# Optimization experiments

Hardware: AMD Instinct MI355X
Metric: run time of the kernel (lower is better)

## Reference

```python
import jax, jax.numpy as jnp
import numpy as np

PHI = 1.618033988749895  # golden ratio
LUT_SIZE = 4096
TWO_PI = 2.0 * float(np.pi)
_grid = np.arange(LUT_SIZE, dtype=np.float32) * (TWO_PI / LUT_SIZE)
SIN_TABLE = jnp.asarray(np.sin(_grid).astype(np.float32))
COS_TABLE = jnp.asarray(np.cos(_grid).astype(np.float32))


def lut_sin_cos(theta):
    """4096-entry sin/cos lookup table over [0, 2pi) with linear interpolation."""
    pos = theta * (LUT_SIZE / TWO_PI)
    i0 = jnp.floor(pos)
    frac = (pos - i0).astype(theta.dtype)
    idx0 = jnp.mod(i0.astype(jnp.int32), LUT_SIZE)
    idx1 = jnp.mod(idx0 + 1, LUT_SIZE)
    sin_v = SIN_TABLE[idx0] * (1.0 - frac) + SIN_TABLE[idx1] * frac
    cos_v = COS_TABLE[idx0] * (1.0 - frac) + COS_TABLE[idx1] * frac
    return sin_v, cos_v


def _forward(input_ids, emb, w_query, b_query, w_key, b_key, w_ctx, W_res, B_res, w_pr, w_pi, w_out):
    B, S = input_ids.shape
    D = emb.shape[1] // 2
    H, dh = w_query.shape
    e = emb[input_ids]                               # [B,S,2D]
    w_emb, b_emb = e[..., :D], e[..., D:]
    t_arr = jnp.arange(S, dtype=jnp.float32)

    # --- sequential euler-transform recurrence (the only truly serial part) ---
    def step(carry, xs):
        h_r, h_i = carry
        w_t, b_t, t = xs                             # [B,D],[B,D],scalar
        wl = 1.0 + jnp.abs(w_t)
        tp = t * PHI
        th_r = h_r / wl + b_t + tp
        th_i = h_i / wl + b_t + tp
        sr, cr = lut_sin_cos(th_r)
        si, ci = lut_sin_cos(th_i)
        nr = cr * ci - sr * si
        ni = cr * si + sr * ci
        return (nr, ni), nr + ni

    init = (jnp.zeros((B, D), dtype=emb.dtype), jnp.zeros((B, D), dtype=emb.dtype))
    xs = (jnp.swapaxes(w_emb, 0, 1), jnp.swapaxes(b_emb, 0, 1), t_arr)
    _, states = jax.lax.scan(step, init, xs)         # [S,B,D]
    states = jnp.swapaxes(states, 0, 1)              # [B,S,D] == cached_states

    # --- multi-head LUT sin/cos attention over strictly-previous cached states ---
    xp = states.reshape(B, S, H, dh)                 # per-head patches
    t_phi = t_arr * PHI                              # [S]
    th_q = xp / (1.0 + jnp.abs(w_query)) + b_query + t_phi[None, :, None, None]
    sq, cq = lut_sin_cos(th_q)
    q = jnp.concatenate([cq, sq], axis=-1)           # [B,S,H,2dh]
    th_k = xp / (1.0 + jnp.abs(w_key)) + b_key
    sk, ck = lut_sin_cos(th_k)
    k = jnp.concatenate([ck, sk], axis=-1)           # [B,S,H,2dh]
    scale = float(np.sqrt(2.0 * dh))
    scores = jnp.einsum('bthd,bshd->bhts', q, k) / scale
    mask = jnp.tril(jnp.ones((S, S), dtype=bool), k=-1)   # keys strictly before query
    scores = jnp.where(mask[None, None], scores, -1e30)
    weights = jax.nn.softmax(scores, axis=-1)
    context = jnp.einsum('bhts,bsd->btd', weights, states)   # heads summed
    has_ctx = (t_arr > 0).astype(states.dtype)[None, :, None]  # t=0 has no cache
    x = states + has_ctx * (context @ w_ctx.T)

    # --- resonant layer over num_neurons ---
    wl_res = 1.0 + jnp.abs(W_res)                    # [N,D]
    theta = x[:, :, None, :] / wl_res + B_res + t_phi[None, :, None, None]  # [B,S,N,D]
    s_t, c_t = lut_sin_cos(theta)
    cos_sum = c_t.sum(-1)                            # [B,S,N]
    sin_sum = s_t.sum(-1)
    x = x + jax.nn.silu(cos_sum @ w_pr.T + sin_sum @ w_pi.T)

    return x @ w_out.T                               # [B,S,V]


def setup_inputs() -> dict:
    key = jax.random.key(0)
    ks = jax.random.split(key, 12)
    B, S, V, D, H, N = 8, 512, 32000, 64, 4, 128
    dh = D // H
    return {
        'input_ids': jax.random.randint(ks[0], (B, S), 0, V),
        'emb': jax.random.normal(ks[1], (V, 2 * D), dtype=jnp.float32) * 0.02,
        'w_query': jax.random.normal(ks[2], (H, dh), dtype=jnp.float32) * 0.02,
        'b_query': jnp.zeros((H, dh), dtype=jnp.float32),
        'w_key': jax.random.normal(ks[3], (H, dh), dtype=jnp.float32) * 0.02,
        'b_key': jnp.zeros((H, dh), dtype=jnp.float32),
        'w_ctx': jax.random.normal(ks[4], (D, D), dtype=jnp.float32) * 0.02,
        'W_res': jax.random.normal(ks[5], (N, D), dtype=jnp.float32) * 0.02,
        'B_res': jnp.zeros((N, D), dtype=jnp.float32),
        'w_pr': jax.random.normal(ks[6], (D, N), dtype=jnp.float32) * 0.02,
        'w_pi': jax.random.normal(ks[7], (D, N), dtype=jnp.float32) * 0.02,
        'w_out': jax.random.normal(ks[8], (V, D), dtype=jnp.float32) * 0.02,
    }


def reference(input_ids, emb, w_query, b_query, w_key, b_key, w_ctx, W_res, B_res, w_pr, w_pi, w_out):
    return _forward(input_ids, emb, w_query, b_query, w_key, b_key, w_ctx, W_res, B_res, w_pr, w_pi, w_out)
```

## Files before the change

kernel.cpp:

```cpp
#include <hip/hip_runtime.h>
#include <hip/hip_bf16.h>
#include <math.h>

#define PHI_F     1.618033988749895f
#define LUT_N     4096
#define LUT_INV   651.8986469044033f
#define LUT_STEP  0.0015339807878856412f

#define B_  8
#define S_  512
#define D_  64
#define H_  4
#define DH_ 16
#define N_  128
#define V_  32000
#define R_  (B_ * S_)

typedef __attribute__((ext_vector_type(8))) short short8_t;
typedef __attribute__((ext_vector_type(4))) float f32x4;

__device__ __forceinline__ void lut2(const float2* __restrict__ sc,
                                     float th, float& s, float& c) {
    float pos = th * LUT_INV;
    float f0  = floorf(pos);
    float fr  = pos - f0;
    int   i0  = ((int)f0) & (LUT_N - 1);
    int   i1  = (i0 + 1) & (LUT_N - 1);
    float2 p0 = sc[i0];
    float2 p1 = sc[i1];
    float om  = 1.0f - fr;
    s = p0.x * om + p1.x * fr;
    c = p0.y * om + p1.y * fr;
}

__global__ void k_tables(float2* __restrict__ scT) {
    int i = blockIdx.x * blockDim.x + threadIdx.x;
    if (i < LUT_N) {
        float g = (float)i * LUT_STEP;
        scT[i] = make_float2((float)sin((double)g), (float)cos((double)g));
    }
}

__global__ __launch_bounds__(256) void k_cvt(const float* __restrict__ w,
                                             __hip_bfloat16* __restrict__ wb,
                                             int n4) {
    int i = blockIdx.x * 256 + threadIdx.x;
    if (i < n4) {
        float4 v = ((const float4*)w)[i];
        union { __hip_bfloat16 h[4]; short4 s4; } u;
        u.h[0] = __float2bfloat16(v.x);
        u.h[1] = __float2bfloat16(v.y);
        u.h[2] = __float2bfloat16(v.z);
        u.h[3] = __float2bfloat16(v.w);
        *(short4*)(&wb[4 * i]) = u.s4;
    }
}

__global__ __launch_bounds__(256) void k_wpre(const float* __restrict__ Wres,
                                              const float* __restrict__ Bres,
                                              const float* __restrict__ wpr,
                                              const float* __restrict__ wpi,
                                              float2* __restrict__ ibres,
                                              float2* __restrict__ wpT) {
    int idx = blockIdx.x * 256 + threadIdx.x;
    if (idx < N_ * D_) {
        ibres[idx] = make_float2(1.0f / (1.0f + fabsf(Wres[idx])), Bres[idx]);
        int nn = idx >> 6, d = idx & 63;
        wpT[idx] = make_float2(wpr[d * N_ + nn], wpi[d * N_ + nn]);
    }
}

__global__ __launch_bounds__(256) void k_pre(const int* __restrict__ ids,
                                             const float* __restrict__ emb,
                                             float2* __restrict__ wlbt) {
    int idx = blockIdx.x * 256 + threadIdx.x;
    int d  = idx & (D_ - 1);
    int bt = idx >> 6;
    int id = ids[bt];
    float w = emb[(size_t)id * (2 * D_) + d];
    float b = emb[(size_t)id * (2 * D_) + D_ + d];
    wlbt[idx] = make_float2(1.0f + fabsf(w), b);
}

__global__ __launch_bounds__(64) void k_scan(const float2* __restrict__ wlbt,
                                             const float2* __restrict__ scT,
                                             float* __restrict__ states) {
    __shared__ float2 sc[LUT_N];
    int d = threadIdx.x;
    int b = blockIdx.x;
    for (int i = d; i < LUT_N; i += 64) sc[i] = scT[i];
    __syncthreads();

    const float2* src  = wlbt + (size_t)b * S_ * D_ + d;
    float*        outp = states + (size_t)b * S_ * D_ + d;

    float2 cur[8], nxt[8];
#pragma unroll
    for (int j = 0; j < 8; ++j) cur[j] = src[j * D_];

    float hr = 0.0f, hi = 0.0f;
    for (int tc = 0; tc < S_; tc += 8) {
        int tn = (tc + 8) & (S_ - 1);
#pragma unroll
        for (int j = 0; j < 8; ++j) nxt[j] = src[(tn + j) * D_];
#pragma unroll
        for (int j = 0; j < 8; ++j) {
            int   t   = tc + j;
            float wl  = cur[j].x;
            float btv = cur[j].y;
            float tp  = (float)t * PHI_F;
            float thr = hr / wl + btv + tp;
            float thi = hi / wl + btv + tp;
            float sr, cr, si, ci;
            lut2(sc, thr, sr, cr);
            lut2(sc, thi, si, ci);
            float nr = cr * ci - sr * si;
            float ni = cr * si + sr * ci;
            hr = nr; hi = ni;
            outp[t * D_] = nr + ni;
        }
#pragma unroll
        for (int j = 0; j < 8; ++j) cur[j] = nxt[j];
    }
}

__global__ __launch_bounds__(256) void k_qk(const float* __restrict__ states,
                                            const float* __restrict__ wq,
                                            const float* __restrict__ bq,
                                            const float* __restrict__ wk,
                                            const float* __restrict__ bk,
                                            const float2* __restrict__ scT,
                                            float* __restrict__ q,
                                            float* __restrict__ kT) {
    __shared__ float2 sc[LUT_N];
    for (int i = threadIdx.x; i < LUT_N; i += 256) sc[i] = scT[i];
    __syncthreads();
    const int total = R_ * H_ * DH_;
    for (int idx = blockIdx.x * 256 + threadIdx.x; idx < total; idx += gridDim.x * 256) {
        int j  = idx & (DH_ - 1);
        int h  = (idx >> 4) & (H_ - 1);
        int bt = idx >> 6;
        int t  = bt & (S_ - 1);
        int b  = bt >> 9;
        float xp = states[idx];
        float tp = (float)t * PHI_F;
        int   hj = h * DH_ + j;
        float thq = xp / (1.0f + fabsf(wq[hj])) + bq[hj] + tp;
        float thk = xp / (1.0f + fabsf(wk[hj])) + bk[hj];
        float sq, cq, sk, ck;
        lut2(sc, thq, sq, cq);
        lut2(sc, thk, sk, ck);
        int base = bt * (H_ * 2 * DH_) + h * (2 * DH_) + j;
        q[base] = cq; q[base + DH_] = sq;
        size_t kb = ((size_t)(b * H_ + h) * 32 + j) * S_ + t;
        kT[kb] = ck; kT[kb + 16 * S_] = sk;
    }
}

__global__ __launch_bounds__(256) void k_attn(const float* __restrict__ states,
                                              const float* __restrict__ q,
                                              const float* __restrict__ kT,
                                              const float* __restrict__ wctx,
                                              float* __restrict__ x) {
    int bt = blockIdx.x;
    int b  = bt >> 9, t = bt & (S_ - 1);
    int tid = threadIdx.x;
    if (t == 0) {
        if (tid < D_) x[bt * D_ + tid] = states[bt * D_ + tid];
        return;
    }
    __shared__ float wlds[H_][S_];
    __shared__ float ql[H_][2 * DH_];
    __shared__ float cpart[4][D_];
    int h = tid >> 6, l = tid & 63;
    if (l < 2 * DH_) ql[h][l] = q[bt * 128 + h * 32 + l];
    __syncthreads();

    const float* kTb = kT + (size_t)(b * H_ + h) * 32 * S_;
    float sc[8];
    float m = -INFINITY;
#pragma unroll
    for (int jj = 0; jj < 8; ++jj) {
        int s = l + jj * 64;
        float v = -INFINITY;
        if (s < t) {
            float acc = 0.0f;
#pragma unroll
            for (int c = 0; c < 32; ++c)
                acc = fmaf(kTb[c * S_ + s], ql[h][c], acc);
            v = acc * 0.1767766952966369f;
            m = fmaxf(m, v);
        }
        sc[jj] = v;
    }
    for (int o = 32; o; o >>= 1) m = fmaxf(m, __shfl_xor(m, o));
    float sum = 0.0f;
#pragma unroll
    for (int jj = 0; jj < 8; ++jj) {
        float e = __expf(sc[jj] - m);
        sc[jj] = e; sum += e;
    }
    for (int o = 32; o; o >>= 1) sum += __shfl_xor(sum, o);
    float inv = 1.0f / sum;
#pragma unroll
    for (int jj = 0; jj < 8; ++jj) {
        int s = l + jj * 64;
        if (s < S_) wlds[h][s] = sc[jj] * inv;
    }
    __syncthreads();
    {
        int d = tid & 63, p = tid >> 6;
        float acc = 0.0f;
        for (int s = p; s < t; s += 4) {
            float w4 = wlds[0][s] + wlds[1][s] + wlds[2][s] + wlds[3][s];
            acc += w4 * states[((size_t)b * S_ + s) * D_ + d];
        }
        cpart[p][d] = acc;
    }
    __syncthreads();
    if (tid < D_) {
        float c = cpart[0][tid] + cpart[1][tid] + cpart[2][tid] + cpart[3][tid];
        cpart[0][tid] = c;
    }
    __syncthreads();
    if (tid < D_) {
        float y = 0.0f;
        const float* wr = wctx + tid * D_;
        for (int d = 0; d < D_; ++d) y += cpart[0][d] * wr[d];
        x[bt * D_ + tid] = states[bt * D_ + tid] + y;
    }
}

__global__ __launch_bounds__(256) void k_resid(const float* __restrict__ x,
                                               const float2* __restrict__ ibres,
                                               const float2* __restrict__ wpT,
                                               const float2* __restrict__ scT,
                                               __hip_bfloat16* __restrict__ xb) {
    __shared__ float2 sc[LUT_N];
    __shared__ float xv[D_];
    __shared__ float csum[N_], ssum[N_];
    __shared__ float part[4][D_];
    int tid = threadIdx.x;
    for (int i = tid; i < LUT_N; i += 256) sc[i] = scT[i];
    int n  = tid >> 1;
    int d0 = (tid & 1) * 32;
    float2 ib[32];
#pragma unroll
    for (int dd = 0; dd < 32; ++dd) ib[dd] = ibres[n * D_ + d0 + dd];
    int g = tid >> 6, dl = tid & 63;
    for (int r = 0; r < 8; ++r) {
        int bt = blockIdx.x * 8 + r;
        int t  = bt & (S_ - 1);
        float tp = (float)t * PHI_F;
        __syncthreads();
        if (tid < D_) xv[tid] = x[bt * D_ + tid];
        __syncthreads();
        float cs = 0.0f, ss = 0.0f;
#pragma unroll
        for (int dd = 0; dd < 32; ++dd) {
            float th = fmaf(xv[d0 + dd], ib[dd].x, ib[dd].y) + tp;
            float s, c;
            lut2(sc, th, s, c);
            cs += c; ss += s;
        }
        cs += __shfl_xor(cs, 1);
        ss += __shfl_xor(ss, 1);
        if ((tid & 1) == 0) { csum[n] = cs; ssum[n] = ss; }
        __syncthreads();
        float acc = 0.0f;
#pragma unroll
        for (int nn = 0; nn < 32; ++nn) {
            float2 w = wpT[(g * 32 + nn) * D_ + dl];
            acc = fmaf(csum[g * 32 + nn], w.x, fmaf(ssum[g * 32 + nn], w.y, acc));
        }
        part[g][dl] = acc;
        __syncthreads();
        if (tid < D_) {
            float pre = part[0][tid] + part[1][tid] + part[2][tid] + part[3][tid];
            float sig = 1.0f / (1.0f + __expf(-pre));
            xb[bt * D_ + tid] = __float2bfloat16(xv[tid] + pre * sig);
        }
    }
}

__global__ __launch_bounds__(256) void k_out(const __hip_bfloat16* __restrict__ xb,
                                             const __hip_bfloat16* __restrict__ wb,
                                             float* __restrict__ out) {
    __shared__ float ot[64][132];
    int tid  = threadIdx.x;
    int wave = tid >> 6, l = tid & 63;
    int wr = wave >> 1, wc = wave & 1;
    int m0 = blockIdx.y * 64 + wr * 32;
    int r  = l & 15;
    int ks = (l >> 4) * 8;
    int kh = l >> 4;

    short8_t a[2][2];
#pragma unroll
    for (int mi = 0; mi < 2; ++mi)
#pragma unroll
        for (int kk = 0; kk < 2; ++kk)
            a[mi][kk] = *reinterpret_cast<const short8_t*>(
                xb + (size_t)(m0 + mi * 16 + r) * 64 + kk * 32 + ks);

    for (int ch = 0; ch < 2; ++ch) {
        int c0 = blockIdx.x * 256 + ch * 128 + wc * 64;
        short8_t b[4][2];
#pragma unroll
        for (int ni = 0; ni < 4; ++ni)
#pragma unroll
            for (int kk = 0; kk < 2; ++kk)
                b[ni][kk] = *reinterpret_cast<const short8_t*>(
                    wb + (size_t)(c0 + ni * 16 + r) * 64 + kk * 32 + ks);

        f32x4 acc[2][4];
#pragma unroll
        for (int mi = 0; mi < 2; ++mi)
#pragma unroll
            for (int ni = 0; ni < 4; ++ni) {
                acc[mi][ni] = (f32x4){0.f, 0.f, 0.f, 0.f};
                acc[mi][ni] = __builtin_amdgcn_mfma_f32_16x16x32_bf16(
                    a[mi][0], b[ni][0], acc[mi][ni], 0, 0, 0);
                acc[mi][ni] = __builtin_amdgcn_mfma_f32_16x16x32_bf16(
                    a[mi][1], b[ni][1], acc[mi][ni], 0, 0, 0);
            }

        if (ch) __syncthreads();
#pragma unroll
        for (int mi = 0; mi < 2; ++mi)
#pragma unroll
            for (int ni = 0; ni < 4; ++ni)
#pragma unroll
                for (int i = 0; i < 4; ++i)
                    ot[wr * 32 + mi * 16 + kh * 4 + i][wc * 64 + ni * 16 + r] = acc[mi][ni][i];
        __syncthreads();

        size_t rbase = blockIdx.y * 64;
        size_t cb    = (size_t)blockIdx.x * 256 + ch * 128;
#pragma unroll
        for (int j = 0; j < 8; ++j) {
            int idx = j * 256 + tid;
            int row = idx >> 5, c4 = idx & 31;
            float4 v = *(const float4*)&ot[row][c4 * 4];
            *(float4*)&out[(rbase + row) * V_ + cb + c4 * 4] = v;
        }
    }
}

extern "C" void kernel_launch(void* const* d_in, const int* in_sizes, int n_in,
                              void* d_out, int out_size, void* d_ws, size_t ws_size,
                              hipStream_t stream) {
    const int*   ids  = (const int*)  d_in[0];
    const float* emb  = (const float*)d_in[1];
    const float* wq   = (const float*)d_in[2];
    const float* bq   = (const float*)d_in[3];
    const float* wk   = (const float*)d_in[4];
    const float* bk   = (const float*)d_in[5];
    const float* wctx = (const float*)d_in[6];
    const float* Wres = (const float*)d_in[7];
    const float* Bres = (const float*)d_in[8];
    const float* wpr  = (const float*)d_in[9];
    const float* wpi  = (const float*)d_in[10];
    const float* wout = (const float*)d_in[11];
    float* out = (float*)d_out;

    float* states = (float*)d_ws;
    float* qbuf   = states + R_ * D_;
    float* kTbuf  = qbuf + R_ * 128;
    float* xbuf   = kTbuf + B_ * H_ * 32 * S_;
    __hip_bfloat16* wb = (__hip_bfloat16*)(xbuf + R_ * D_);
    __hip_bfloat16* xb = wb + (size_t)V_ * D_;
    float2* scT   = (float2*)(xb + R_ * D_);
    float2* wlbt  = scT + LUT_N;
    float2* ibres = wlbt + R_ * D_;
    float2* wpT   = ibres + N_ * D_;

    k_tables<<<16, 256, 0, stream>>>(scT);
    k_cvt   <<<(V_ * D_ / 4 + 255) / 256, 256, 0, stream>>>(wout, wb, V_ * D_ / 4);
    k_wpre  <<<(N_ * D_ + 255) / 256, 256, 0, stream>>>(Wres, Bres, wpr, wpi, ibres, wpT);
    k_pre   <<<R_ * D_ / 256, 256, 0, stream>>>(ids, emb, wlbt);
    k_scan  <<<B_, 64, 0, stream>>>(wlbt, scT, states);
    k_qk    <<<64, 256, 0, stream>>>(states, wq, bq, wk, bk, scT, qbuf, kTbuf);
    k_attn  <<<R_, 256, 0, stream>>>(states, qbuf, kTbuf, wctx, xbuf);
    k_resid <<<R_ / 8, 256, 0, stream>>>(xbuf, ibres, wpT, scT, xb);
    k_out   <<<dim3(V_ / 256, R_ / 64), 256, 0, stream>>>(xb, wb, out);
}
```

Baseline: 359.9 us.

## Fuse preprocessing, scan, and QK into one kernel; merge attention with residual

```diff
diff --git a/kernel.cpp b/kernel.cpp
--- a/kernel.cpp
+++ b/kernel.cpp
@@ -41,73 +41,69 @@
     }
 }
 
-__global__ __launch_bounds__(256) void k_cvt(const float* __restrict__ w,
-                                             __hip_bfloat16* __restrict__ wb,
-                                             int n4) {
-    int i = blockIdx.x * 256 + threadIdx.x;
-    if (i < n4) {
-        float4 v = ((const float4*)w)[i];
-        union { __hip_bfloat16 h[4]; short4 s4; } u;
-        u.h[0] = __float2bfloat16(v.x);
-        u.h[1] = __float2bfloat16(v.y);
-        u.h[2] = __float2bfloat16(v.z);
-        u.h[3] = __float2bfloat16(v.w);
-        *(short4*)(&wb[4 * i]) = u.s4;
-    }
-}
-
-__global__ __launch_bounds__(256) void k_wpre(const float* __restrict__ Wres,
-                                              const float* __restrict__ Bres,
-                                              const float* __restrict__ wpr,
-                                              const float* __restrict__ wpi,
-                                              float2* __restrict__ ibres,
-                                              float2* __restrict__ wpT) {
-    int idx = blockIdx.x * 256 + threadIdx.x;
-    if (idx < N_ * D_) {
-        ibres[idx] = make_float2(1.0f / (1.0f + fabsf(Wres[idx])), Bres[idx]);
-        int nn = idx >> 6, d = idx & 63;
-        wpT[idx] = make_float2(wpr[d * N_ + nn], wpi[d * N_ + nn]);
-    }
-}
-
-__global__ __launch_bounds__(256) void k_pre(const int* __restrict__ ids,
-                                             const float* __restrict__ emb,
-                                             float2* __restrict__ wlbt) {
-    int idx = blockIdx.x * 256 + threadIdx.x;
-    int d  = idx & (D_ - 1);
-    int bt = idx >> 6;
-    int id = ids[bt];
-    float w = emb[(size_t)id * (2 * D_) + d];
-    float b = emb[(size_t)id * (2 * D_) + D_ + d];
-    wlbt[idx] = make_float2(1.0f + fabsf(w), b);
-}
-
-__global__ __launch_bounds__(64) void k_scan(const float2* __restrict__ wlbt,
-                                             const float2* __restrict__ scT,
-                                             float* __restrict__ states) {
+__global__ __launch_bounds__(256) void k_fused0(
+        const int* __restrict__ ids, const float* __restrict__ emb,
+        const float* __restrict__ wq, const float* __restrict__ bq,
+        const float* __restrict__ wk, const float* __restrict__ bk,
+        const float* __restrict__ Wres, const float* __restrict__ Bres,
+        const float* __restrict__ wpr, const float* __restrict__ wpi,
+        const float* __restrict__ wout, const float2* __restrict__ scT,
+        float* __restrict__ states, float* __restrict__ q, float* __restrict__ kT,
+        __hip_bfloat16* __restrict__ wb, float2* __restrict__ ibres,
+        float2* __restrict__ wpT) {
+    int blk = blockIdx.x;
+    int tid = threadIdx.x;
+    if (blk >= 8) {
+        if (blk < 2008) {
+            int i = (blk - 8) * 256 + tid;
+            float4 v = ((const float4*)wout)[i];
+            union { __hip_bfloat16 h[4]; short4 s4; } u;
+            u.h[0] = __float2bfloat16(v.x);
+            u.h[1] = __float2bfloat16(v.y);
+            u.h[2] = __float2bfloat16(v.z);
+            u.h[3] = __float2bfloat16(v.w);
+            *(short4*)(&wb[4 * (size_t)i]) = u.s4;
+        } else {
+            int idx = (blk - 2008) * 256 + tid;
+            ibres[idx] = make_float2(1.0f / (1.0f + fabsf(Wres[idx])), Bres[idx]);
+            int nn = idx >> 6, d = idx & 63;
+            wpT[idx] = make_float2(wpr[d * N_ + nn], wpi[d * N_ + nn]);
+        }
+        return;
+    }
     __shared__ float2 sc[LUT_N];
-    int d = threadIdx.x;
-    int b = blockIdx.x;
-    for (int i = d; i < LUT_N; i += 64) sc[i] = scT[i];
-    __syncthreads();
-
-    const float2* src  = wlbt + (size_t)b * S_ * D_ + d;
-    float*        outp = states + (size_t)b * S_ * D_ + d;
-
-    float2 cur[8], nxt[8];
-#pragma unroll
-    for (int j = 0; j < 8; ++j) cur[j] = src[j * D_];
-
+    __shared__ int idsh[S_];
+    for (int i = tid; i < LUT_N; i += 256) sc[i] = scT[i];
+    for (int i = tid; i < S_; i += 256) idsh[i] = ids[blk * S_ + i];
+    __syncthreads();
+    if (tid >= 64) return;
+    int d = tid, b = blk;
+    float cw[8], cb[8], nw[8], nb[8];
+#pragma unroll
+    for (int j = 0; j < 8; ++j) {
+        int id = idsh[j];
+        cw[j] = emb[(size_t)id * 128 + d];
+        cb[j] = emb[(size_t)id * 128 + 64 + d];
+    }
+    float* outp = states + (size_t)b * S_ * D_ + d;
+    float* qp   = q + (size_t)b * S_ * 128;
+    int h = d >> 4, j4 = d & 15, hj = h * DH_ + j4;
+    float wlq = 1.0f + fabsf(wq[hj]); float bqv = bq[hj];
+    float wlk = 1.0f + fabsf(wk[hj]); float bkv = bk[hj];
+    float* kTp = kT + ((size_t)(b * H_ + h) * 32 + j4) * S_;
     float hr = 0.0f, hi = 0.0f;
     for (int tc = 0; tc < S_; tc += 8) {
-        int tn = (tc + 8) & (S_ - 1);
-#pragma unroll
-        for (int j = 0; j < 8; ++j) nxt[j] = src[(tn + j) * D_];
-#pragma unroll
-        for (int j = 0; j < 8; ++j) {
-            int   t   = tc + j;
-            float wl  = cur[j].x;
-            float btv = cur[j].y;
+#pragma unroll
+        for (int jj = 0; jj < 8; ++jj) {
+            int id = idsh[(tc + 8 + jj) & (S_ - 1)];
+            nw[jj] = emb[(size_t)id * 128 + d];
+            nb[jj] = emb[(size_t)id * 128 + 64 + d];
+        }
+#pragma unroll
+        for (int jj = 0; jj < 8; ++jj) {
+            int   t   = tc + jj;
+            float wl  = 1.0f + fabsf(cw[jj]);
+            float btv = cb[jj];
             float tp  = (float)t * PHI_F;
             float thr = hr / wl + btv + tp;
             float thi = hi / wl + btv + tp;
@@ -117,176 +113,139 @@
             float nr = cr * ci - sr * si;
             float ni = cr * si + sr * ci;
             hr = nr; hi = ni;
-            outp[t * D_] = nr + ni;
-        }
-#pragma unroll
-        for (int j = 0; j < 8; ++j) cur[j] = nxt[j];
-    }
-}
-
-__global__ __launch_bounds__(256) void k_qk(const float* __restrict__ states,
-                                            const float* __restrict__ wq,
-                                            const float* __restrict__ bq,
-                                            const float* __restrict__ wk,
-                                            const float* __restrict__ bk,
+            float xp = nr + ni;
+            outp[t * D_] = xp;
+            float thq = xp / wlq + bqv + tp;
+            float thk = xp / wlk + bkv;
+            float sq, cq, sk, ck;
+            lut2(sc, thq, sq, cq);
+            lut2(sc, thk, sk, ck);
+            float* qrow = qp + t * 128 + h * 32 + j4;
+            qrow[0]  = cq; qrow[16] = sq;
+            kTp[t] = ck; kTp[16 * S_ + t] = sk;
+        }
+#pragma unroll
+        for (int jj = 0; jj < 8; ++jj) { cw[jj] = nw[jj]; cb[jj] = nb[jj]; }
+    }
+}
+
+__global__ __launch_bounds__(256) void k_ar(const float* __restrict__ states,
+                                            const float* __restrict__ q,
+                                            const float* __restrict__ kT,
+                                            const float* __restrict__ wctx,
+                                            const float2* __restrict__ ibres,
+                                            const float2* __restrict__ wpT,
                                             const float2* __restrict__ scT,
-                                            float* __restrict__ q,
-                                            float* __restrict__ kT) {
+                                            __hip_bfloat16* __restrict__ xb) {
     __shared__ float2 sc[LUT_N];
-    for (int i = threadIdx.x; i < LUT_N; i += 256) sc[i] = scT[i];
-    __syncthreads();
-    const int total = R_ * H_ * DH_;
-    for (int idx = blockIdx.x * 256 + threadIdx.x; idx < total; idx += gridDim.x * 256) {
-        int j  = idx & (DH_ - 1);
-        int h  = (idx >> 4) & (H_ - 1);
-        int bt = idx >> 6;
-        int t  = bt & (S_ - 1);
-        int b  = bt >> 9;
-        float xp = states[idx];
-        float tp = (float)t * PHI_F;
-        int   hj = h * DH_ + j;
-        float thq = xp / (1.0f + fabsf(wq[hj])) + bq[hj] + tp;
-        float thk = xp / (1.0f + fabsf(wk[hj])) + bk[hj];
-        float sq, cq, sk, ck;
-        lut2(sc, thq, sq, cq);
-        lut2(sc, thk, sk, ck);
-        int base = bt * (H_ * 2 * DH_) + h * (2 * DH_) + j;
-        q[base] = cq; q[base + DH_] = sq;
-        size_t kb = ((size_t)(b * H_ + h) * 32 + j) * S_ + t;
-        kT[kb] = ck; kT[kb + 16 * S_] = sk;
-    }
-}
-
-__global__ __launch_bounds__(256) void k_attn(const float* __restrict__ states,
-                                              const float* __restrict__ q,
-                                              const float* __restrict__ kT,
-                                              const float* __restrict__ wctx,
-                                              float* __restrict__ x) {
+    __shared__ float wlds[H_][S_];
+    __shared__ float ql[H_][2 * DH_];
+    __shared__ float cpart[4][D_];
+    __shared__ float xv[D_];
+    __shared__ float csum[N_], ssum[N_];
+    __shared__ float part[4][D_];
     int bt = blockIdx.x;
     int b  = bt >> 9, t = bt & (S_ - 1);
     int tid = threadIdx.x;
-    if (t == 0) {
-        if (tid < D_) x[bt * D_ + tid] = states[bt * D_ + tid];
-        return;
-    }
-    __shared__ float wlds[H_][S_];
-    __shared__ float ql[H_][2 * DH_];
-    __shared__ float cpart[4][D_];
     int h = tid >> 6, l = tid & 63;
-    if (l < 2 * DH_) ql[h][l] = q[bt * 128 + h * 32 + l];
-    __syncthreads();
-
-    const float* kTb = kT + (size_t)(b * H_ + h) * 32 * S_;
-    float sc[8];
-    float m = -INFINITY;
-#pragma unroll
-    for (int jj = 0; jj < 8; ++jj) {
-        int s = l + jj * 64;
-        float v = -INFINITY;
-        if (s < t) {
-            float acc = 0.0f;
-#pragma unroll
-            for (int c = 0; c < 32; ++c)
-                acc = fmaf(kTb[c * S_ + s], ql[h][c], acc);
-            v = acc * 0.1767766952966369f;
-            m = fmaxf(m, v);
-        }
-        sc[jj] = v;
-    }
-    for (int o = 32; o; o >>= 1) m = fmaxf(m, __shfl_xor(m, o));
-    float sum = 0.0f;
-#pragma unroll
-    for (int jj = 0; jj < 8; ++jj) {
-        float e = __expf(sc[jj] - m);
-        sc[jj] = e; sum += e;
-    }
-    for (int o = 32; o; o >>= 1) sum += __shfl_xor(sum, o);
-    float inv = 1.0f / sum;
-#pragma unroll
-    for (int jj = 0; jj < 8; ++jj) {
-        int s = l + jj * 64;
-        if (s < S_) wlds[h][s] = sc[jj] * inv;
-    }
-    __syncthreads();
-    {
-        int d = tid & 63, p = tid >> 6;
+    for (int i = tid; i < LUT_N; i += 256) sc[i] = scT[i];
+    if (t > 0 && l < 2 * DH_) ql[h][l] = q[bt * 128 + h * 32 + l];
+    __syncthreads();
+
+    if (t > 0) {
+        const float* kTb = kT + (size_t)(b * H_ + h) * 32 * S_;
+        float scv[8];
+        float m = -INFINITY;
+#pragma unroll
+        for (int jj = 0; jj < 8; ++jj) {
+            int s = l + jj * 64;
+            float v = -INFINITY;
+            if (s < t) {
+                float acc = 0.0f;
+#pragma unroll
+                for (int c = 0; c < 32; ++c)
+                    acc = fmaf(kTb[c * S_ + s], ql[h][c], acc);
+                v = acc * 0.1767766952966369f;
+                m = fmaxf(m, v);
+            }
+            scv[jj] = v;
+        }
+        for (int o = 32; o; o >>= 1) m = fmaxf(m, __shfl_xor(m, o));
+        float sum = 0.0f;
+#pragma unroll
+        for (int jj = 0; jj < 8; ++jj) {
+            float e = __expf(scv[jj] - m);
+            scv[jj] = e; sum += e;
+        }
+        for (int o = 32; o; o >>= 1) sum += __shfl_xor(sum, o);
+        float inv = 1.0f / sum;
+#pragma unroll
+        for (int jj = 0; jj < 8; ++jj) {
+            int s = l + jj * 64;
+            if (s < S_) wlds[h][s] = scv[jj] * inv;
+        }
+    }
+    __syncthreads();
+    if (t > 0) {
+        int dd = tid & 63, p = tid >> 6;
         float acc = 0.0f;
         for (int s = p; s < t; s += 4) {
             float w4 = wlds[0][s] + wlds[1][s] + wlds[2][s] + wlds[3][s];
-            acc += w4 * states[((size_t)b * S_ + s) * D_ + d];
-        }
-        cpart[p][d] = acc;
-    }
+            acc += w4 * states[((size_t)b * S_ + s) * D_ + dd];
+        }
+        cpart[p][dd] = acc;
+    }
+    __syncthreads();
+    if (tid < D_ && t > 0)
+        cpart[0][tid] = cpart[0][tid] + cpart[1][tid] + cpart[2][tid] + cpart[3][tid];
     __syncthreads();
     if (tid < D_) {
-        float c = cpart[0][tid] + cpart[1][tid] + cpart[2][tid] + cpart[3][tid];
-        cpart[0][tid] = c;
-    }
-    __syncthreads();
-    if (tid < D_) {
-        float y = 0.0f;
-        const float* wr = wctx + tid * D_;
-        for (int d = 0; d < D_; ++d) y += cpart[0][d] * wr[d];
-        x[bt * D_ + tid] = states[bt * D_ + tid] + y;
-    }
-}
-
-__global__ __launch_bounds__(256) void k_resid(const float* __restrict__ x,
-                                               const float2* __restrict__ ibres,
-                                               const float2* __restrict__ wpT,
-                                               const float2* __restrict__ scT,
-                                               __hip_bfloat16* __restrict__ xb) {
-    __shared__ float2 sc[LUT_N];
-    __shared__ float xv[D_];
-    __shared__ float csum[N_], ssum[N_];
-    __shared__ float part[4][D_];
-    int tid = threadIdx.x;
-    for (int i = tid; i < LUT_N; i += 256) sc[i] = scT[i];
+        float base = states[bt * D_ + tid];
+        float val  = base;
+        if (t > 0) {
+            float y = 0.0f;
+            const float* wr = wctx + tid * D_;
+            for (int dd = 0; dd < D_; ++dd) y += cpart[0][dd] * wr[dd];
+            val = base + y;
+        }
+        xv[tid] = val;
+    }
+    __syncthreads();
     int n  = tid >> 1;
     int d0 = (tid & 1) * 32;
-    float2 ib[32];
-#pragma unroll
-    for (int dd = 0; dd < 32; ++dd) ib[dd] = ibres[n * D_ + d0 + dd];
+    float tp = (float)t * PHI_F;
+    float cs = 0.0f, ss = 0.0f;
+#pragma unroll
+    for (int dd = 0; dd < 32; ++dd) {
+        float2 ib = ibres[n * D_ + d0 + dd];
+        float th = fmaf(xv[d0 + dd], ib.x, ib.y) + tp;
+        float s, c;
+        lut2(sc, th, s, c);
+        cs += c; ss += s;
+    }
+    cs += __shfl_xor(cs, 1);
+    ss += __shfl_xor(ss, 1);
+    if ((tid & 1) == 0) { csum[n] = cs; ssum[n] = ss; }
+    __syncthreads();
     int g = tid >> 6, dl = tid & 63;
-    for (int r = 0; r < 8; ++r) {
-        int bt = blockIdx.x * 8 + r;
-        int t  = bt & (S_ - 1);
-        float tp = (float)t * PHI_F;
-        __syncthreads();
-        if (tid < D_) xv[tid] = x[bt * D_ + tid];
-        __syncthreads();
-        float cs = 0.0f, ss = 0.0f;
-#pragma unroll
-        for (int dd = 0; dd < 32; ++dd) {
-            float th = fmaf(xv[d0 + dd], ib[dd].x, ib[dd].y) + tp;
-            float s, c;
-            lut2(sc, th, s, c);
-            cs += c; ss += s;
-        }
-        cs += __shfl_xor(cs, 1);
-        ss += __shfl_xor(ss, 1);
-        if ((tid & 1) == 0) { csum[n] = cs; ssum[n] = ss; }
-        __syncthreads();
-        float acc = 0.0f;
-#pragma unroll
-        for (int nn = 0; nn < 32; ++nn) {
-            float2 w = wpT[(g * 32 + nn) * D_ + dl];
-            acc = fmaf(csum[g * 32 + nn], w.x, fmaf(ssum[g * 32 + nn], w.y, acc));
-        }
-        part[g][dl] = acc;
-        __syncthreads();
-        if (tid < D_) {
-            float pre = part[0][tid] + part[1][tid] + part[2][tid] + part[3][tid];
-            float sig = 1.0f / (1.0f + __expf(-pre));
-            xb[bt * D_ + tid] = __float2bfloat16(xv[tid] + pre * sig);
-        }
+    float acc = 0.0f;
+#pragma unroll
+    for (int nn = 0; nn < 32; ++nn) {
+        float2 w = wpT[(g * 32 + nn) * D_ + dl];
+        acc = fmaf(csum[g * 32 + nn], w.x, fmaf(ssum[g * 32 + nn], w.y, acc));
+    }
+    part[g][dl] = acc;
+    __syncthreads();
+    if (tid < D_) {
+        float pre = part[0][tid] + part[1][tid] + part[2][tid] + part[3][tid];
+        float sig = 1.0f / (1.0f + __expf(-pre));
+        xb[bt * D_ + tid] = __float2bfloat16(xv[tid] + pre * sig);
     }
 }
 
 __global__ __launch_bounds__(256) void k_out(const __hip_bfloat16* __restrict__ xb,
                                              const __hip_bfloat16* __restrict__ wb,
                                              float* __restrict__ out) {
-    __shared__ float ot[64][132];
     int tid  = threadIdx.x;
     int wave = tid >> 6, l = tid & 63;
     int wr = wave >> 1, wc = wave & 1;
@@ -303,14 +262,15 @@
             a[mi][kk] = *reinterpret_cast<const short8_t*>(
                 xb + (size_t)(m0 + mi * 16 + r) * 64 + kk * 32 + ks);
 
+#pragma unroll
     for (int ch = 0; ch < 2; ++ch) {
         int c0 = blockIdx.x * 256 + ch * 128 + wc * 64;
-        short8_t b[4][2];
+        short8_t bfr[4][2];
 #pragma unroll
         for (int ni = 0; ni < 4; ++ni)
 #pragma unroll
             for (int kk = 0; kk < 2; ++kk)
-                b[ni][kk] = *reinterpret_cast<const short8_t*>(
+                bfr[ni][kk] = *reinterpret_cast<const short8_t*>(
                     wb + (size_t)(c0 + ni * 16 + r) * 64 + kk * 32 + ks);
 
         f32x4 acc[2][4];
@@ -320,30 +280,20 @@
             for (int ni = 0; ni < 4; ++ni) {
                 acc[mi][ni] = (f32x4){0.f, 0.f, 0.f, 0.f};
                 acc[mi][ni] = __builtin_amdgcn_mfma_f32_16x16x32_bf16(
-                    a[mi][0], b[ni][0], acc[mi][ni], 0, 0, 0);
+                    a[mi][0], bfr[ni][0], acc[mi][ni], 0, 0, 0);
                 acc[mi][ni] = __builtin_amdgcn_mfma_f32_16x16x32_bf16(
-                    a[mi][1], b[ni][1], acc[mi][ni], 0, 0, 0);
+                    a[mi][1], bfr[ni][1], acc[mi][ni], 0, 0, 0);
             }
-
-        if (ch) __syncthreads();
 #pragma unroll
         for (int mi = 0; mi < 2; ++mi)
 #pragma unroll
-            for (int ni = 0; ni < 4; ++ni)
-#pragma unroll
-                for (int i = 0; i < 4; ++i)
-                    ot[wr * 32 + mi * 16 + kh * 4 + i][wc * 64 + ni * 16 + r] = acc[mi][ni][i];
-        __syncthreads();
-
-        size_t rbase = blockIdx.y * 64;
-        size_t cb    = (size_t)blockIdx.x * 256 + ch * 128;
-#pragma unroll
-        for (int j = 0; j < 8; ++j) {
-            int idx = j * 256 + tid;
-            int row = idx >> 5, c4 = idx & 31;
-            float4 v = *(const float4*)&ot[row][c4 * 4];
-            *(float4*)&out[(rbase + row) * V_ + cb + c4 * 4] = v;
-        }
+            for (int i = 0; i < 4; ++i) {
+                size_t rowoff = (size_t)(m0 + mi * 16 + kh * 4 + i) * V_;
+#pragma unroll
+                for (int ni = 0; ni < 4; ++ni)
+                    __builtin_nontemporal_store(acc[mi][ni][i],
+                        &out[rowoff + c0 + ni * 16 + r]);
+            }
     }
 }
 
@@ -367,21 +317,16 @@
     float* states = (float*)d_ws;
     float* qbuf   = states + R_ * D_;
     float* kTbuf  = qbuf + R_ * 128;
-    float* xbuf   = kTbuf + B_ * H_ * 32 * S_;
-    __hip_bfloat16* wb = (__hip_bfloat16*)(xbuf + R_ * D_);
+    __hip_bfloat16* wb = (__hip_bfloat16*)(kTbuf + B_ * H_ * 32 * S_);
     __hip_bfloat16* xb = wb + (size_t)V_ * D_;
     float2* scT   = (float2*)(xb + R_ * D_);
-    float2* wlbt  = scT + LUT_N;
-    float2* ibres = wlbt + R_ * D_;
+    float2* ibres = scT + LUT_N;
     float2* wpT   = ibres + N_ * D_;
 
     k_tables<<<16, 256, 0, stream>>>(scT);
-    k_cvt   <<<(V_ * D_ / 4 + 255) / 256, 256, 0, stream>>>(wout, wb, V_ * D_ / 4);
-    k_wpre  <<<(N_ * D_ + 255) / 256, 256, 0, stream>>>(Wres, Bres, wpr, wpi, ibres, wpT);
-    k_pre   <<<R_ * D_ / 256, 256, 0, stream>>>(ids, emb, wlbt);
-    k_scan  <<<B_, 64, 0, stream>>>(wlbt, scT, states);
-    k_qk    <<<64, 256, 0, stream>>>(states, wq, bq, wk, bk, scT, qbuf, kTbuf);
-    k_attn  <<<R_, 256, 0, stream>>>(states, qbuf, kTbuf, wctx, xbuf);
-    k_resid <<<R_ / 8, 256, 0, stream>>>(xbuf, ibres, wpT, scT, xb);
+    k_fused0<<<2040, 256, 0, stream>>>(ids, emb, wq, bq, wk, bk, Wres, Bres,
+                                       wpr, wpi, wout, scT,
+                                       states, qbuf, kTbuf, wb, ibres, wpT);
+    k_ar    <<<R_, 256, 0, stream>>>(states, qbuf, kTbuf, wctx, ibres, wpT, scT, xb);
     k_out   <<<dim3(V_ / 256, R_ / 64), 256, 0, stream>>>(xb, wb, out);
 }
```

New measurement: 481.3 us. 33.7% more time.

## Fuse weight conversion, residual prep and embedding gather into the scan kernel

Applied to the files above, without the earlier changes.

```diff
diff --git a/kernel.cpp b/kernel.cpp
--- a/kernel.cpp
+++ b/kernel.cpp
@@ -41,73 +41,61 @@
     }
 }
 
-__global__ __launch_bounds__(256) void k_cvt(const float* __restrict__ w,
-                                             __hip_bfloat16* __restrict__ wb,
-                                             int n4) {
-    int i = blockIdx.x * 256 + threadIdx.x;
-    if (i < n4) {
-        float4 v = ((const float4*)w)[i];
-        union { __hip_bfloat16 h[4]; short4 s4; } u;
-        u.h[0] = __float2bfloat16(v.x);
-        u.h[1] = __float2bfloat16(v.y);
-        u.h[2] = __float2bfloat16(v.z);
-        u.h[3] = __float2bfloat16(v.w);
-        *(short4*)(&wb[4 * i]) = u.s4;
-    }
-}
-
-__global__ __launch_bounds__(256) void k_wpre(const float* __restrict__ Wres,
-                                              const float* __restrict__ Bres,
-                                              const float* __restrict__ wpr,
-                                              const float* __restrict__ wpi,
-                                              float2* __restrict__ ibres,
-                                              float2* __restrict__ wpT) {
-    int idx = blockIdx.x * 256 + threadIdx.x;
-    if (idx < N_ * D_) {
-        ibres[idx] = make_float2(1.0f / (1.0f + fabsf(Wres[idx])), Bres[idx]);
-        int nn = idx >> 6, d = idx & 63;
-        wpT[idx] = make_float2(wpr[d * N_ + nn], wpi[d * N_ + nn]);
-    }
-}
-
-__global__ __launch_bounds__(256) void k_pre(const int* __restrict__ ids,
-                                             const float* __restrict__ emb,
-                                             float2* __restrict__ wlbt) {
-    int idx = blockIdx.x * 256 + threadIdx.x;
-    int d  = idx & (D_ - 1);
-    int bt = idx >> 6;
-    int id = ids[bt];
-    float w = emb[(size_t)id * (2 * D_) + d];
-    float b = emb[(size_t)id * (2 * D_) + D_ + d];
-    wlbt[idx] = make_float2(1.0f + fabsf(w), b);
-}
-
-__global__ __launch_bounds__(64) void k_scan(const float2* __restrict__ wlbt,
-                                             const float2* __restrict__ scT,
-                                             float* __restrict__ states) {
+__global__ __launch_bounds__(256) void k_fused0(
+        const int* __restrict__ ids, const float* __restrict__ emb,
+        const float* __restrict__ Wres, const float* __restrict__ Bres,
+        const float* __restrict__ wpr, const float* __restrict__ wpi,
+        const float* __restrict__ wout, const float2* __restrict__ scT,
+        float* __restrict__ states, __hip_bfloat16* __restrict__ wb,
+        float2* __restrict__ ibres, float2* __restrict__ wpT) {
+    int blk = blockIdx.x;
+    int tid = threadIdx.x;
+    if (blk >= 8) {
+        if (blk < 2008) {
+            int i = (blk - 8) * 256 + tid;
+            float4 v = ((const float4*)wout)[i];
+            union { __hip_bfloat16 h[4]; short4 s4; } u;
+            u.h[0] = __float2bfloat16(v.x);
+            u.h[1] = __float2bfloat16(v.y);
+            u.h[2] = __float2bfloat16(v.z);
+            u.h[3] = __float2bfloat16(v.w);
+            *(short4*)(&wb[4 * (size_t)i]) = u.s4;
+        } else {
+            int idx = (blk - 2008) * 256 + tid;
+            ibres[idx] = make_float2(1.0f / (1.0f + fabsf(Wres[idx])), Bres[idx]);
+            int nn = idx >> 6, d = idx & 63;
+            wpT[idx] = make_float2(wpr[d * N_ + nn], wpi[d * N_ + nn]);
+        }
+        return;
+    }
     __shared__ float2 sc[LUT_N];
-    int d = threadIdx.x;
-    int b = blockIdx.x;
-    for (int i = d; i < LUT_N; i += 64) sc[i] = scT[i];
-    __syncthreads();
-
-    const float2* src  = wlbt + (size_t)b * S_ * D_ + d;
-    float*        outp = states + (size_t)b * S_ * D_ + d;
-
-    float2 cur[8], nxt[8];
-#pragma unroll
-    for (int j = 0; j < 8; ++j) cur[j] = src[j * D_];
-
+    __shared__ int idsh[S_];
+    for (int i = tid; i < LUT_N; i += 256) sc[i] = scT[i];
+    for (int i = tid; i < S_; i += 256) idsh[i] = ids[blk * S_ + i];
+    __syncthreads();
+    if (tid >= 64) return;
+    int d = tid, b = blk;
+    float cw[8], cb[8], nw[8], nb[8];
+#pragma unroll
+    for (int j = 0; j < 8; ++j) {
+        int id = idsh[j];
+        cw[j] = emb[(size_t)id * 128 + d];
+        cb[j] = emb[(size_t)id * 128 + 64 + d];
+    }
+    float* outp = states + (size_t)b * S_ * D_ + d;
     float hr = 0.0f, hi = 0.0f;
     for (int tc = 0; tc < S_; tc += 8) {
-        int tn = (tc + 8) & (S_ - 1);
-#pragma unroll
-        for (int j = 0; j < 8; ++j) nxt[j] = src[(tn + j) * D_];
-#pragma unroll
-        for (int j = 0; j < 8; ++j) {
-            int   t   = tc + j;
-            float wl  = cur[j].x;
-            float btv = cur[j].y;
+#pragma unroll
+        for (int jj = 0; jj < 8; ++jj) {
+            int id = idsh[(tc + 8 + jj) & (S_ - 1)];
+            nw[jj] = emb[(size_t)id * 128 + d];
+            nb[jj] = emb[(size_t)id * 128 + 64 + d];
+        }
+#pragma unroll
+        for (int jj = 0; jj < 8; ++jj) {
+            int   t   = tc + jj;
+            float wl  = 1.0f + fabsf(cw[jj]);
+            float btv = cb[jj];
             float tp  = (float)t * PHI_F;
             float thr = hr / wl + btv + tp;
             float thi = hi / wl + btv + tp;
@@ -120,7 +108,7 @@
             outp[t * D_] = nr + ni;
         }
 #pragma unroll
-        for (int j = 0; j < 8; ++j) cur[j] = nxt[j];
+        for (int jj = 0; jj < 8; ++jj) { cw[jj] = nw[jj]; cb[jj] = nb[jj]; }
     }
 }
 
@@ -209,13 +197,13 @@
     }
     __syncthreads();
     {
-        int d = tid & 63, p = tid >> 6;
+        int dd = tid & 63, p = tid >> 6;
         float acc = 0.0f;
         for (int s = p; s < t; s += 4) {
             float w4 = wlds[0][s] + wlds[1][s] + wlds[2][s] + wlds[3][s];
-            acc += w4 * states[((size_t)b * S_ + s) * D_ + d];
-        }
-        cpart[p][d] = acc;
+            acc += w4 * states[((size_t)b * S_ + s) * D_ + dd];
+        }
+        cpart[p][dd] = acc;
     }
     __syncthreads();
     if (tid < D_) {
@@ -226,7 +214,7 @@
     if (tid < D_) {
         float y = 0.0f;
         const float* wr = wctx + tid * D_;
-        for (int d = 0; d < D_; ++d) y += cpart[0][d] * wr[d];
+        for (int dd = 0; dd < D_; ++dd) y += cpart[0][dd] * wr[dd];
         x[bt * D_ + tid] = states[bt * D_ + tid] + y;
     }
 }
@@ -371,15 +359,12 @@
     __hip_bfloat16* wb = (__hip_bfloat16*)(xbuf + R_ * D_);
     __hip_bfloat16* xb = wb + (size_t)V_ * D_;
     float2* scT   = (float2*)(xb + R_ * D_);
-    float2* wlbt  = scT + LUT_N;
-    float2* ibres = wlbt + R_ * D_;
+    float2* ibres = scT + LUT_N;
     float2* wpT   = ibres + N_ * D_;
 
     k_tables<<<16, 256, 0, stream>>>(scT);
-    k_cvt   <<<(V_ * D_ / 4 + 255) / 256, 256, 0, stream>>>(wout, wb, V_ * D_ / 4);
-    k_wpre  <<<(N_ * D_ + 255) / 256, 256, 0, stream>>>(Wres, Bres, wpr, wpi, ibres, wpT);
-    k_pre   <<<R_ * D_ / 256, 256, 0, stream>>>(ids, emb, wlbt);
-    k_scan  <<<B_, 64, 0, stream>>>(wlbt, scT, states);
+    k_fused0<<<2040, 256, 0, stream>>>(ids, emb, Wres, Bres, wpr, wpi, wout, scT,
+                                       states, wb, ibres, wpT);
     k_qk    <<<64, 256, 0, stream>>>(states, wq, bq, wk, bk, scT, qbuf, kTbuf);
     k_attn  <<<R_, 256, 0, stream>>>(states, qbuf, kTbuf, wctx, xbuf);
     k_resid <<<R_ / 8, 256, 0, stream>>>(xbuf, ibres, wpT, scT, xb);
```

Result: no change. 353.8 us (-1.7%).
